# Optimization experiments

Hardware: AMD Instinct MI355X
Metric: run time of the kernel (lower is better)

## Reference

```python
import jax, jax.numpy as jnp
import numpy as np

WINDOW = 256   # init kwarg window_size
CAUSAL = False # init kwarg causal


def setup_inputs() -> dict:
    key = jax.random.key(0)
    k1, k2, k3 = jax.random.split(key, 3)
    shape = (2, 16, 4096, 64)  # (batch, heads, seq_len, head_dim); seq_len % WINDOW == 0
    return {
        "query": jax.random.normal(k1, shape, dtype=jnp.float32),
        "key": jax.random.normal(k2, shape, dtype=jnp.float32),
        "value": jax.random.normal(k3, shape, dtype=jnp.float32),
    }


def _neighbor_blocks(x, nb, W):
    # x: [B,H,S,D] -> [B,H,nb,3W,D] where block n holds key blocks n-1,n,n+1 (zero padded at ends)
    B, H, S, D = x.shape
    xb = x.reshape(B, H, nb, W, D)
    xp = jnp.pad(xb, ((0, 0), (0, 0), (1, 1), (0, 0), (0, 0)))
    return jnp.concatenate([xp[:, :, j:j + nb] for j in range(3)], axis=3)


def _swa(query, key, value, window, causal):
    B, H, S, D = query.shape
    W = window
    nb = S // W
    scale = jnp.float32(1.0 / np.sqrt(D))
    qb = query.reshape(B, H, nb, W, D)
    kb = _neighbor_blocks(key, nb, W)    # [B,H,nb,3W,D]
    vb = _neighbor_blocks(value, nb, W)  # [B,H,nb,3W,D]

    # band mask: query global pos qi = n*W + q, key global pos ki = n*W + (k - W)
    qpos = jnp.arange(W)[:, None]              # [W,1]
    kpos = jnp.arange(3 * W)[None, :] - W      # [1,3W] relative block offset
    diff = kpos - qpos                         # [W,3W] == ki - qi
    ki = jnp.arange(nb)[:, None, None] * W + kpos[None]  # [nb,1,3W]
    valid = (ki >= 0) & (ki < S)
    if causal:
        band = (diff >= -W) & (diff <= 0)
    else:
        band = jnp.abs(diff) <= W
    mask = valid & band[None]                  # [nb,W,3W]

    scores = jnp.einsum('bhnqd,bhnkd->bhnqk', qb, kb) * scale  # [B,H,nb,W,3W]
    scores = jnp.where(mask, scores, -jnp.inf)
    attn = jax.nn.softmax(scores, axis=-1)
    out = jnp.einsum('bhnqk,bhnkd->bhnqd', attn, vb)
    return out.reshape(B, H, S, D)


def reference(query, key, value):
    return _swa(query, key, value, WINDOW, CAUSAL)
```

## Files before the change

### kernel.cpp

```cpp
#include <hip/hip_runtime.h>
#include <hip/hip_bf16.h>

typedef __attribute__((ext_vector_type(4)))  float f32x4;
typedef __attribute__((ext_vector_type(16))) float f32x16;
typedef __attribute__((ext_vector_type(8)))  short bf16x8;
typedef __attribute__((ext_vector_type(4)))  unsigned u32x4;

#define S_LEN 4096
#define HEAD_D 64
#define WIN 256
#define QBLK 128
#define KVBLK 64
#define KSTR 72
#define VSTR 72
#define QSCALE 0.18033688f

#define KBYTES (KVBLK * KSTR * 2)
#define VBYTES (HEAD_D * VSTR * 2)
#define LPAR_OFF (2 * KBYTES + 2 * VBYTES)
#define SMEM_BYTES (LPAR_OFF + 2 * 4 * 32 * 4)

static __device__ __forceinline__ unsigned cvt2(float lo, float hi) {
  unsigned r;
  asm("v_cvt_pk_bf16_f32 %0, %1, %2" : "=v"(r) : "v"(lo), "v"(hi));
  return r;
}

__global__ __launch_bounds__(512, 4)
void swa_fwd(const float* __restrict__ Q, const float* __restrict__ K,
             const float* __restrict__ V, float* __restrict__ O) {
  __shared__ __attribute__((aligned(16))) char smem[SMEM_BYTES];

  const int tid  = threadIdx.x;
  const int widx = tid >> 6;
  const int lane = tid & 63;
  const int hi   = lane >> 5;
  const int c    = lane & 31;
  const int qg   = widx & 3;
  const int kh   = widx >> 2;
  const int kho  = kh * 32;

  const int pb  = blockIdx.x;
  const int bh  = (pb & 7) * 4 + ((pb >> 3) >> 5);
  const int qb  = (pb >> 3) & 31;
  const int bq0 = qb * QBLK;
  const int q0w = bq0 + qg * 32;

  const size_t base = (size_t)bh * S_LEN * HEAD_D;
  const float* Qp = Q + base;
  const float* Kp = K + base;
  const float* Vp = V + base;
  float*       Op = O + base;

  const f32x16 Z16 = {0.f,0.f,0.f,0.f,0.f,0.f,0.f,0.f,0.f,0.f,0.f,0.f,0.f,0.f,0.f,0.f};

  bf16x8 aq[4];
  {
    const float* qr = Qp + (size_t)(q0w + c) * HEAD_D + hi * 8;
    #pragma unroll
    for (int ch = 0; ch < 4; ++ch) {
      f32x4 x0 = *(const f32x4*)(qr + ch * 16);
      f32x4 x1 = *(const f32x4*)(qr + ch * 16 + 4);
      u32x4 au;
      au[0] = cvt2(x0[0] * QSCALE, x0[1] * QSCALE);
      au[1] = cvt2(x0[2] * QSCALE, x0[3] * QSCALE);
      au[2] = cvt2(x1[0] * QSCALE, x1[1] * QSCALE);
      au[3] = cvt2(x1[2] * QSCALE, x1[3] * QSCALE);
      aq[ch] = __builtin_bit_cast(bf16x8, au);
    }
  }

  f32x16 acc0 = Z16, acc1 = Z16;
  float lsum = 0.f;

  const int lo   = max(0, bq0 - WIN);
  const int khiB = min(S_LEN, bq0 + QBLK + WIN);
  const int nt   = (khiB - lo) >> 6;

  const int krow  = tid >> 3;
  const int kc8   = (tid & 7) << 3;
  const int key2  = (tid & 31) << 1;
  const int key2p = (key2 & ~12) | ((key2 & 4) << 1) | ((key2 & 8) >> 1);
  const int vd4   = (tid >> 5) << 2;
  const float* kpt  = Kp + (size_t)(lo + krow) * HEAD_D + kc8;
  const float* vpt0 = Vp + (size_t)(lo + key2) * HEAD_D + vd4;
  const float* vpt1 = vpt0 + HEAD_D;

  f32x4 ka0, ka1, va0, va1;
  #define LOAD_TILE() do {                         \
    ka0 = *(const f32x4*)kpt;                      \
    ka1 = *(const f32x4*)(kpt + 4);                \
    va0 = *(const f32x4*)vpt0;                     \
    va1 = *(const f32x4*)vpt1;                     \
    kpt  += KVBLK * HEAD_D;                        \
    vpt0 += KVBLK * HEAD_D;                        \
    vpt1 += KVBLK * HEAD_D;                        \
  } while (0)

  #define STAGE_TO(buf) do {                                              \
    short* kb_ = (short*)(smem + (buf) * KBYTES);                         \
    short* vb_ = (short*)(smem + 2 * KBYTES + (buf) * VBYTES);            \
    u32x4 kw;                                                             \
    kw[0] = cvt2(ka0[0], ka0[1]);                                         \
    kw[1] = cvt2(ka0[2], ka0[3]);                                         \
    kw[2] = cvt2(ka1[0], ka1[1]);                                         \
    kw[3] = cvt2(ka1[2], ka1[3]);                                         \
    *(u32x4*)&kb_[krow * KSTR + kc8] = kw;                                \
    _Pragma("unroll")                                                     \
    for (int j = 0; j < 4; ++j)                                           \
      *(unsigned*)&vb_[(vd4 + j) * VSTR + key2p] = cvt2(va0[j], va1[j]);  \
  } while (0)

  LOAD_TILE();
  STAGE_TO(0);
  LOAD_TILE();
  __syncthreads();

  int cur = 0;
  for (int t = 0; t < nt; ++t) {
    const int kv0 = lo + (t << 6);
    const short* kb = (const short*)(smem + cur * KBYTES);
    const short* vb = (const short*)(smem + 2 * KBYTES + cur * VBYTES);

    f32x16 s = Z16;
    __builtin_amdgcn_s_setprio(1);
    #pragma unroll
    for (int ch = 0; ch < 4; ++ch) {
      bf16x8 akf = *(const bf16x8*)&kb[(kho + c) * KSTR + ch * 16 + hi * 8];
      s = __builtin_amdgcn_mfma_f32_32x32x16_bf16(akf, aq[ch], s, 0, 0, 0);
    }
    __builtin_amdgcn_s_setprio(0);

    const int rel = kv0 + kho - q0w;
    if (rel >= -224 && rel <= 224) {
      #pragma unroll
      for (int g = 0; g < 16; ++g) {
        const float p = exp2f(s[g]);
        s[g] = p; lsum += p;
      }
    } else {
      const int bm = rel + 4 * hi - c + WIN;
      #pragma unroll
      for (int g = 0; g < 16; ++g) {
        const int ro = (g & 3) + 8 * (g >> 2);
        const float p = ((unsigned)(bm + ro) <= 2u * WIN) ? exp2f(s[g]) : 0.f;
        s[g] = p; lsum += p;
      }
    }

    __builtin_amdgcn_s_setprio(1);
    #pragma unroll
    for (int kt = 0; kt < 2; ++kt) {
      u32x4 pau;
      #pragma unroll
      for (int p2 = 0; p2 < 4; ++p2)
        pau[p2] = cvt2(s[kt * 8 + 2 * p2], s[kt * 8 + 2 * p2 + 1]);
      const bf16x8 pa = __builtin_bit_cast(bf16x8, pau);
      const int vo = kho + kt * 16 + hi * 8;
      bf16x8 bv0 = *(const bf16x8*)&vb[c * VSTR + vo];
      acc0 = __builtin_amdgcn_mfma_f32_32x32x16_bf16(pa, bv0, acc0, 0, 0, 0);
      bf16x8 bv1 = *(const bf16x8*)&vb[(32 + c) * VSTR + vo];
      acc1 = __builtin_amdgcn_mfma_f32_32x32x16_bf16(pa, bv1, acc1, 0, 0, 0);
    }
    __builtin_amdgcn_s_setprio(0);

    if (t + 1 < nt) {
      STAGE_TO(cur ^ 1);
      if (t + 2 < nt) LOAD_TILE();
      __syncthreads();
    }
    cur ^= 1;
  }

  lsum += __shfl_xor(lsum, 32);
  __syncthreads();
  float* o_mrg = (float*)smem;
  float* l_par = (float*)(smem + LPAR_OFF);
  if (hi == 0) l_par[(kh * 4 + qg) * 32 + c] = lsum;
  if (kh == 0) {
    #pragma unroll
    for (int g = 0; g < 16; ++g) {
      const int qrow = (g & 3) + 8 * (g >> 2) + 4 * hi;
      o_mrg[(qg * 32 + qrow) * HEAD_D + c]      = acc0[g];
      o_mrg[(qg * 32 + qrow) * HEAD_D + 32 + c] = acc1[g];
    }
  }
  __syncthreads();
  if (kh == 1) {
    if (hi == 0) l_par[qg * 32 + c] = 1.0f / (l_par[qg * 32 + c] + l_par[(4 + qg) * 32 + c]);
    __asm__ volatile("s_waitcnt lgkmcnt(0)" ::: "memory");
    __builtin_amdgcn_sched_barrier(0);
    #pragma unroll
    for (int g = 0; g < 16; ++g) {
      const int qrow = (g & 3) + 8 * (g >> 2) + 4 * hi;
      const float iv = l_par[qg * 32 + qrow];
      float* orow = Op + (size_t)(q0w + qrow) * HEAD_D;
      orow[c]      = (o_mrg[(qg * 32 + qrow) * HEAD_D + c]      + acc0[g]) * iv;
      orow[32 + c] = (o_mrg[(qg * 32 + qrow) * HEAD_D + 32 + c] + acc1[g]) * iv;
    }
  }
}

extern "C" void kernel_launch(void* const* d_in, const int* in_sizes, int n_in,
                              void* d_out, int out_size, void* d_ws, size_t ws_size,
                              hipStream_t stream) {
  const float* q = (const float*)d_in[0];
  const float* k = (const float*)d_in[1];
  const float* v = (const float*)d_in[2];
  float* o = (float*)d_out;
  const int blocks = 2 * 16 * (S_LEN / QBLK);
  swa_fwd<<<dim3(blocks), dim3(512), 0, stream>>>(q, k, v, o);
}
```

Measured before the change: 52.20 us.

## Give each wave private K/V loading and skip tiles outside the band

Drops the block-wide shared double-buffered K/V staging. Each wave now loads its own K fragments straight from global memory into registers and converts them to bf16 there, and transposes its own V slice into a per-wave LDS region. This removes the __syncthreads in the main loop and lets each wave skip K/V tiles that lie entirely outside its window band. It also splits the softmax row sum into two accumulators, uses the raw exp2 builtin, and lowers launch bounds to 2 blocks per SIMD. In exchange, each K/V element is fetched separately by the waves that need it (redundant global traffic), register pressure rises, and there is less latency hiding.

Result: slower. 139.0 us (+166.3%).

```diff
diff --git a/kernel.cpp b/kernel.cpp
--- a/kernel.cpp
+++ b/kernel.cpp
@@ -11,13 +11,11 @@
 #define WIN 256
 #define QBLK 128
 #define KVBLK 64
-#define KSTR 72
-#define VSTR 72
+#define VSTR 40
 #define QSCALE 0.18033688f
 
-#define KBYTES (KVBLK * KSTR * 2)
-#define VBYTES (HEAD_D * VSTR * 2)
-#define LPAR_OFF (2 * KBYTES + 2 * VBYTES)
+#define VWBYTES (HEAD_D * VSTR * 2)
+#define LPAR_OFF (8 * VWBYTES)
 #define SMEM_BYTES (LPAR_OFF + 2 * 4 * 32 * 4)
 
 static __device__ __forceinline__ unsigned cvt2(float lo, float hi) {
@@ -26,7 +24,7 @@
   return r;
 }
 
-__global__ __launch_bounds__(512, 4)
+__global__ __launch_bounds__(512, 2)
 void swa_fwd(const float* __restrict__ Q, const float* __restrict__ K,
              const float* __restrict__ V, float* __restrict__ O) {
   __shared__ __attribute__((aligned(16))) char smem[SMEM_BYTES];
@@ -71,107 +69,130 @@
   }
 
   f32x16 acc0 = Z16, acc1 = Z16;
-  float lsum = 0.f;
+  float lsA = 0.f, lsB = 0.f;
 
   const int lo   = max(0, bq0 - WIN);
   const int khiB = min(S_LEN, bq0 + QBLK + WIN);
   const int nt   = (khiB - lo) >> 6;
 
-  const int krow  = tid >> 3;
-  const int kc8   = (tid & 7) << 3;
-  const int key2  = (tid & 31) << 1;
-  const int key2p = (key2 & ~12) | ((key2 & 4) << 1) | ((key2 & 8) >> 1);
-  const int vd4   = (tid >> 5) << 2;
-  const float* kpt  = Kp + (size_t)(lo + krow) * HEAD_D + kc8;
-  const float* vpt0 = Vp + (size_t)(lo + key2) * HEAD_D + vd4;
-  const float* vpt1 = vpt0 + HEAD_D;
-
-  f32x4 ka0, ka1, va0, va1;
-  #define LOAD_TILE() do {                         \
-    ka0 = *(const f32x4*)kpt;                      \
-    ka1 = *(const f32x4*)(kpt + 4);                \
-    va0 = *(const f32x4*)vpt0;                     \
-    va1 = *(const f32x4*)vpt1;                     \
-    kpt  += KVBLK * HEAD_D;                        \
-    vpt0 += KVBLK * HEAD_D;                        \
-    vpt1 += KVBLK * HEAD_D;                        \
+  short* const vw = (short*)(smem + widx * VWBYTES);
+  const short* const vrd = vw + c * VSTR + hi * 8;
+
+  const int kp   = lane & 15;
+  const int dg   = lane >> 4;
+  const int key2 = kp << 1;
+  const int kp2p = (key2 & ~12) | ((key2 & 4) << 1) | ((key2 & 8) >> 1);
+  short* const vwr = vw + dg * 16 * VSTR + kp2p;
+
+  unsigned kbase = (unsigned)(lo + kho + c) * HEAD_D + hi * 8;
+  unsigned vbase = (unsigned)(lo + kho + key2) * HEAD_D + dg * 16;
+
+  f32x4 kfa[4], kfb[4];
+  f32x4 va0, va1, va2, va3;
+  f32x4 vb0, vb1, vb2, vb3;
+
+  #define LOAD_KF() do {                                          \
+    _Pragma("unroll")                                             \
+    for (int ch = 0; ch < 4; ++ch) {                              \
+      kfa[ch] = *(const f32x4*)(Kp + kbase + ch * 16);            \
+      kfb[ch] = *(const f32x4*)(Kp + kbase + ch * 16 + 4);        \
+    }                                                             \
   } while (0)
 
-  #define STAGE_TO(buf) do {                                              \
-    short* kb_ = (short*)(smem + (buf) * KBYTES);                         \
-    short* vb_ = (short*)(smem + 2 * KBYTES + (buf) * VBYTES);            \
-    u32x4 kw;                                                             \
-    kw[0] = cvt2(ka0[0], ka0[1]);                                         \
-    kw[1] = cvt2(ka0[2], ka0[3]);                                         \
-    kw[2] = cvt2(ka1[0], ka1[1]);                                         \
-    kw[3] = cvt2(ka1[2], ka1[3]);                                         \
-    *(u32x4*)&kb_[krow * KSTR + kc8] = kw;                                \
-    _Pragma("unroll")                                                     \
-    for (int j = 0; j < 4; ++j)                                           \
-      *(unsigned*)&vb_[(vd4 + j) * VSTR + key2p] = cvt2(va0[j], va1[j]);  \
+  #define LOAD_VF() do {                                          \
+    va0 = *(const f32x4*)(Vp + vbase);                            \
+    va1 = *(const f32x4*)(Vp + vbase + 4);                        \
+    va2 = *(const f32x4*)(Vp + vbase + 8);                        \
+    va3 = *(const f32x4*)(Vp + vbase + 12);                       \
+    vb0 = *(const f32x4*)(Vp + vbase + HEAD_D);                   \
+    vb1 = *(const f32x4*)(Vp + vbase + HEAD_D + 4);               \
+    vb2 = *(const f32x4*)(Vp + vbase + HEAD_D + 8);               \
+    vb3 = *(const f32x4*)(Vp + vbase + HEAD_D + 12);              \
   } while (0)
 
-  LOAD_TILE();
-  STAGE_TO(0);
-  LOAD_TILE();
-  __syncthreads();
-
-  int cur = 0;
+  #define WRITE_VF() do {                                                         \
+    _Pragma("unroll")                                                             \
+    for (int i = 0; i < 4; ++i) *(unsigned*)&vwr[i * VSTR]        = cvt2(va0[i], vb0[i]); \
+    _Pragma("unroll")                                                             \
+    for (int i = 0; i < 4; ++i) *(unsigned*)&vwr[(4 + i) * VSTR]  = cvt2(va1[i], vb1[i]); \
+    _Pragma("unroll")                                                             \
+    for (int i = 0; i < 4; ++i) *(unsigned*)&vwr[(8 + i) * VSTR]  = cvt2(va2[i], vb2[i]); \
+    _Pragma("unroll")                                                             \
+    for (int i = 0; i < 4; ++i) *(unsigned*)&vwr[(12 + i) * VSTR] = cvt2(va3[i], vb3[i]); \
+  } while (0)
+
+  {
+    const int rel0 = lo + kho - q0w;
+    if (rel0 >= -287 && rel0 <= 287) {
+      LOAD_VF();
+      WRITE_VF();
+    }
+    vbase += KVBLK * HEAD_D;
+  }
+
   for (int t = 0; t < nt; ++t) {
-    const int kv0 = lo + (t << 6);
-    const short* kb = (const short*)(smem + cur * KBYTES);
-    const short* vb = (const short*)(smem + 2 * KBYTES + cur * VBYTES);
+    const int rel   = lo + (t << 6) + kho - q0w;
+    const bool live  = (rel >= -287) && (rel <= 287);
+    const bool liveN = (t + 1 < nt) && (rel + 64 >= -287) && (rel + 64 <= 287);
 
     f32x16 s = Z16;
-    __builtin_amdgcn_s_setprio(1);
-    #pragma unroll
-    for (int ch = 0; ch < 4; ++ch) {
-      bf16x8 akf = *(const bf16x8*)&kb[(kho + c) * KSTR + ch * 16 + hi * 8];
-      s = __builtin_amdgcn_mfma_f32_32x32x16_bf16(akf, aq[ch], s, 0, 0, 0);
-    }
-    __builtin_amdgcn_s_setprio(0);
-
-    const int rel = kv0 + kho - q0w;
-    if (rel >= -224 && rel <= 224) {
+    if (live) {
+      LOAD_KF();
+      __builtin_amdgcn_s_setprio(1);
       #pragma unroll
-      for (int g = 0; g < 16; ++g) {
-        const float p = exp2f(s[g]);
-        s[g] = p; lsum += p;
+      for (int ch = 0; ch < 4; ++ch) {
+        u32x4 au;
+        au[0] = cvt2(kfa[ch][0], kfa[ch][1]);
+        au[1] = cvt2(kfa[ch][2], kfa[ch][3]);
+        au[2] = cvt2(kfb[ch][0], kfb[ch][1]);
+        au[3] = cvt2(kfb[ch][2], kfb[ch][3]);
+        const bf16x8 akf = __builtin_bit_cast(bf16x8, au);
+        s = __builtin_amdgcn_mfma_f32_32x32x16_bf16(akf, aq[ch], s, 0, 0, 0);
       }
-    } else {
-      const int bm = rel + 4 * hi - c + WIN;
+      __builtin_amdgcn_s_setprio(0);
+    }
+    if (liveN) LOAD_VF();
+
+    if (live) {
+      if (rel >= -224 && rel <= 224) {
+        #pragma unroll
+        for (int g = 0; g < 16; g += 2) {
+          const float p0 = __builtin_amdgcn_exp2f(s[g]);
+          const float p1 = __builtin_amdgcn_exp2f(s[g + 1]);
+          s[g] = p0; s[g + 1] = p1; lsA += p0; lsB += p1;
+        }
+      } else {
+        const int bm = rel + 4 * hi - c + WIN;
+        #pragma unroll
+        for (int g = 0; g < 16; ++g) {
+          const int ro = (g & 3) + 8 * (g >> 2);
+          const float p = ((unsigned)(bm + ro) <= 2u * WIN)
+                            ? __builtin_amdgcn_exp2f(s[g]) : 0.f;
+          s[g] = p; if (g & 1) lsB += p; else lsA += p;
+        }
+      }
+      __builtin_amdgcn_s_setprio(1);
       #pragma unroll
-      for (int g = 0; g < 16; ++g) {
-        const int ro = (g & 3) + 8 * (g >> 2);
-        const float p = ((unsigned)(bm + ro) <= 2u * WIN) ? exp2f(s[g]) : 0.f;
-        s[g] = p; lsum += p;
+      for (int kt = 0; kt < 2; ++kt) {
+        u32x4 pau;
+        #pragma unroll
+        for (int p2 = 0; p2 < 4; ++p2)
+          pau[p2] = cvt2(s[kt * 8 + 2 * p2], s[kt * 8 + 2 * p2 + 1]);
+        const bf16x8 pa = __builtin_bit_cast(bf16x8, pau);
+        bf16x8 bv0 = *(const bf16x8*)&vrd[kt * 16];
+        acc0 = __builtin_amdgcn_mfma_f32_32x32x16_bf16(pa, bv0, acc0, 0, 0, 0);
+        bf16x8 bv1 = *(const bf16x8*)&vrd[kt * 16 + 32 * VSTR];
+        acc1 = __builtin_amdgcn_mfma_f32_32x32x16_bf16(pa, bv1, acc1, 0, 0, 0);
       }
-    }
-
-    __builtin_amdgcn_s_setprio(1);
-    #pragma unroll
-    for (int kt = 0; kt < 2; ++kt) {
-      u32x4 pau;
-      #pragma unroll
-      for (int p2 = 0; p2 < 4; ++p2)
-        pau[p2] = cvt2(s[kt * 8 + 2 * p2], s[kt * 8 + 2 * p2 + 1]);
-      const bf16x8 pa = __builtin_bit_cast(bf16x8, pau);
-      const int vo = kho + kt * 16 + hi * 8;
-      bf16x8 bv0 = *(const bf16x8*)&vb[c * VSTR + vo];
-      acc0 = __builtin_amdgcn_mfma_f32_32x32x16_bf16(pa, bv0, acc0, 0, 0, 0);
-      bf16x8 bv1 = *(const bf16x8*)&vb[(32 + c) * VSTR + vo];
-      acc1 = __builtin_amdgcn_mfma_f32_32x32x16_bf16(pa, bv1, acc1, 0, 0, 0);
-    }
-    __builtin_amdgcn_s_setprio(0);
-
-    if (t + 1 < nt) {
-      STAGE_TO(cur ^ 1);
-      if (t + 2 < nt) LOAD_TILE();
-      __syncthreads();
-    }
-    cur ^= 1;
-  }
-
+      __builtin_amdgcn_s_setprio(0);
+    }
+
+    if (liveN) WRITE_VF();
+    kbase += KVBLK * HEAD_D;
+    vbase += KVBLK * HEAD_D;
+  }
+
+  float lsum = lsA + lsB;
   lsum += __shfl_xor(lsum, 32);
   __syncthreads();
   float* o_mrg = (float*)smem;
```
